# Kernel tuning notes

Hardware: AMD Instinct MI355X
Metric: run time of the kernel (lower is better)

## Reference

```python
import jax, jax.numpy as jnp
import numpy as np

N_HEADS = 16

def setup_inputs() -> dict:
    key = jax.random.key(0)
    ks = jax.random.split(key, 5)
    C = 1024
    B, T = 2, 2048
    s_in = 1.0 / np.sqrt(C)
    x = jax.random.normal(ks[0], (B, T, C), dtype=jnp.float32)
    W_qkv = jax.random.normal(ks[1], (C, 3 * C), dtype=jnp.float32) * s_in
    b_qkv = jnp.zeros((3 * C,), dtype=jnp.float32)
    W_proj = jax.random.normal(ks[2], (C, C), dtype=jnp.float32) * s_in
    b_proj = jnp.zeros((C,), dtype=jnp.float32)
    return {"x": x, "W_qkv": W_qkv, "b_qkv": b_qkv, "W_proj": W_proj, "b_proj": b_proj}

def reference(x, W_qkv, b_qkv, W_proj, b_proj):
    B, T, C = x.shape
    H = N_HEADS
    D = C // H  # head dim
    qkv = x @ W_qkv + b_qkv                      # [B,T,3C]
    q, k, v = jnp.split(qkv, 3, axis=-1)
    # [B,T,C] -> [B,H,T,D]
    q = q.reshape(B, T, H, D).transpose(0, 2, 1, 3)
    k = k.reshape(B, T, H, D).transpose(0, 2, 1, 3)
    v = v.reshape(B, T, H, D).transpose(0, 2, 1, 3)
    scale = 1.0 / np.sqrt(D)
    att = jnp.einsum('bhqd,bhkd->bhqk', q, k) * scale  # [B,H,T,T]
    causal = jnp.tril(jnp.ones((T, T), dtype=bool))
    att = jnp.where(causal[None, None], att, -jnp.inf)
    att = jax.nn.softmax(att, axis=-1)
    y = jnp.einsum('bhqk,bhkd->bhqd', att, v)    # [B,H,T,D]
    y = y.transpose(0, 2, 1, 3).reshape(B, T, C)
    return y @ W_proj + b_proj
```

## Files before the change

kernel.cpp:

```cpp
#include <hip/hip_runtime.h>
#include <hip/hip_bf16.h>
#include <stdint.h>

#define DEVI __device__ __forceinline__

#define BARRIER_FENCED() asm volatile("s_barrier" ::: "memory")
#define WAIT_VM_BARRIER(n) \
  asm volatile("s_waitcnt vmcnt(" #n ")\n\ts_barrier" ::: "memory")

typedef __attribute__((ext_vector_type(8))) short bf16x8;
typedef __attribute__((ext_vector_type(4))) float f32x4;
typedef __attribute__((ext_vector_type(4))) short short4v;
typedef __attribute__((ext_vector_type(4))) float float4v;
typedef __attribute__((ext_vector_type(2))) unsigned int uint2v;

#define QSCALE 0.1803368801111204f

DEVI unsigned short f2bf(float f) {
  union { float f; unsigned u; } v; v.f = f;
  unsigned r = v.u + 0x7FFFu + ((v.u >> 16) & 1u);
  return (unsigned short)(r >> 16);
}

DEVI float bf2f(unsigned short u) {
  union { unsigned u; float f; } v; v.u = ((unsigned)u) << 16; return v.f;
}

DEVI unsigned cvt_pk_bf16(float lo, float hi) {
  unsigned r;
  asm("v_cvt_pk_bf16_f32 %0, %1, %2" : "=v"(r) : "v"(lo), "v"(hi));
  return r;
}

DEVI void async16(unsigned short* lds, const unsigned short* g) {
  __builtin_amdgcn_global_load_lds(
      (const __attribute__((address_space(1))) void*)g,
      (__attribute__((address_space(3))) void*)lds, 16, 0, 0);
}

DEVI int xcd_swz_flat() {
  int orig = (int)blockIdx.x + (int)gridDim.x * (int)blockIdx.y;
  int cpx = ((int)gridDim.x * (int)gridDim.y) >> 3;
  return (orig & 7) * cpx + (orig >> 3);
}

__device__ const signed char TTX[8][3] = {
  {15,15, 0},{ 7,13, 1},{14,12, 2},{14,10, 3},
  {13,10, 8},{ 6, 9, 9},{12,11, 8},{11, 5, 4}};
__device__ const signed char TTS[8][3] = {
  {0,1,2},{2,0,2},{0,0,2},{1,0,2},{1,1,0},{2,0,1},{1,0,1},{1,2,2}};

__global__ void k_prep(const float* __restrict__ x, unsigned short* __restrict__ xb,
                       const float* __restrict__ Wq, const float* __restrict__ Wp,
                       unsigned short* __restrict__ WqT, unsigned short* __restrict__ WpT) {
  __shared__ float tile[32][33];
  const int id = (int)blockIdx.x;
  if (id < 4096) {
    int i = id * 256 + (int)threadIdx.x;
    float4v f = *reinterpret_cast<const float4v*>(x + (size_t)i * 4);
    short4v o;
#pragma unroll
    for (int j = 0; j < 4; ++j) o[j] = (short)f2bf(f[j]);
    *reinterpret_cast<short4v*>(xb + (size_t)i * 4) = o;
    return;
  }
  const int flat = id - 4096;
  const int bx = flat & 127, k0 = (flat >> 7) * 32;
  const float* W;
  unsigned short* Wt;
  int N, n0;
  if (bx < 96) { W = Wq; Wt = WqT; N = 3072; n0 = bx * 32; }
  else         { W = Wp; Wt = WpT; N = 1024; n0 = (bx - 96) * 32; }
  const int K = 1024;
  int r = threadIdx.x >> 5, c = threadIdx.x & 31;
#pragma unroll
  for (int i = 0; i < 4; ++i)
    tile[r + i * 8][c] = W[(size_t)(k0 + r + i * 8) * N + n0 + c];
  __syncthreads();
#pragma unroll
  for (int i = 0; i < 4; ++i)
    Wt[(size_t)(n0 + r + i * 8) * K + k0 + c] = f2bf(tile[c][r + i * 8]);
}

DEVI void stage_ab(unsigned short* AsB, unsigned short* BsB,
                   const unsigned short* Ab, const unsigned short* Bb,
                   int K, int k0, int tid) {
  int row = tid >> 2, cc = (tid & 3) * 8;
  async16(&AsB[tid * 8], Ab + (size_t)row * K + k0 + cc);
  async16(&BsB[tid * 8], Bb + (size_t)row * K + k0 + cc);
}

__global__ __launch_bounds__(512)
void k_gemm(const unsigned short* __restrict__ A,
            const unsigned short* __restrict__ Bt,
            const float* __restrict__ bias,
            unsigned short* __restrict__ qkv,
            unsigned short* __restrict__ vt,
            int M, int N, int K) {
  __shared__ __align__(16) unsigned short As[2][128 * 32];
  __shared__ __align__(16) unsigned short Bs[2][128 * 32];
  const int tid = threadIdx.x;
  const int swzf = xcd_swz_flat();
  const int m0 = (swzf / (int)gridDim.x) * 128, n0 = (swzf % (int)gridDim.x) * 128;
  const int lane = tid & 63, w = tid >> 6;
  const int wr = (w >> 2) * 64, wc = (w & 3) * 32;
  const int lr = lane & 15, lg = lane >> 4;
  f32x4 acc[4][2] = {};
  const unsigned short* Ab = A + (size_t)m0 * K;
  const unsigned short* Bb = Bt + (size_t)n0 * K;

  const int ns = K >> 5;
  stage_ab(As[0], Bs[0], Ab, Bb, K, 0, tid);
  stage_ab(As[1], Bs[1], Ab, Bb, K, 32, tid);
  WAIT_VM_BARRIER(2);
  __builtin_amdgcn_sched_barrier(0);

  for (int s = 0; s < ns; ++s) {
    const int cur = s & 1;
    bf16x8 af[4], bfr[2];
#pragma unroll
    for (int m = 0; m < 4; ++m)
      af[m] = *reinterpret_cast<const bf16x8*>(&As[cur][(wr + m * 16 + lr) * 32 + lg * 8]);
#pragma unroll
    for (int n = 0; n < 2; ++n)
      bfr[n] = *reinterpret_cast<const bf16x8*>(&Bs[cur][(wc + n * 16 + lr) * 32 + lg * 8]);
#pragma unroll
    for (int m = 0; m < 4; ++m)
#pragma unroll
      for (int n = 0; n < 2; ++n)
        acc[m][n] = __builtin_amdgcn_mfma_f32_16x16x32_bf16(af[m], bfr[n], acc[m][n], 0, 0, 0);
    BARRIER_FENCED();
    const int ks = (s + 2 < ns) ? (s + 2) * 32 : 0;
    stage_ab(As[cur], Bs[cur], Ab, Bb, K, ks, tid);
    WAIT_VM_BARRIER(2);
    __builtin_amdgcn_sched_barrier(0);
  }
#pragma unroll
  for (int n = 0; n < 2; ++n) {
    int col = n0 + wc + n * 16 + lr;
    float bv = bias[col];
    int sel = col >> 10, cc = col & 1023;
    int h = cc >> 6, d = cc & 63;
    if (sel < 2) {
      float sc = (sel == 0) ? QSCALE : 1.0f;
#pragma unroll
      for (int m = 0; m < 4; ++m) {
#pragma unroll
        for (int r = 0; r < 4; ++r) {
          int row = m0 + wr + m * 16 + lg * 4 + r;
          int bh = ((row >> 11) << 4) + h;
          int t = row & 2047;
          qkv[((size_t)(sel * 32 + bh) * 2048 + t) * 64 + d] = f2bf((acc[m][n][r] + bv) * sc);
        }
      }
    } else {
#pragma unroll
      for (int m = 0; m < 4; ++m) {
        int row0 = m0 + wr + m * 16 + lg * 4;
        int bh = ((row0 >> 11) << 4) + h;
        int t0 = row0 & 2047;
        short4v pk;
#pragma unroll
        for (int r = 0; r < 4; ++r) pk[r] = (short)f2bf(acc[m][n][r] + bv);
        *reinterpret_cast<short4v*>(&vt[((size_t)(bh * 64 + d)) * 2048 + t0]) = pk;
      }
    }
  }
}

__global__ __launch_bounds__(256)
void k_gemmP(const unsigned short* __restrict__ A,
             const unsigned short* __restrict__ Bt,
             const float* __restrict__ bias,
             float* __restrict__ O, int M, int N, int K) {
  __shared__ __align__(16) unsigned short As[2][64 * 32];
  __shared__ __align__(16) unsigned short Bs[2][64 * 32];
  const int tid = threadIdx.x;
  const int swzf = xcd_swz_flat();
  const int m0 = (swzf / (int)gridDim.x) * 64, n0 = (swzf % (int)gridDim.x) * 64;
  const int lane = tid & 63, w = tid >> 6;
  const int wr = (w >> 1) * 32, wc = (w & 1) * 32;
  const int lr = lane & 15, lg = lane >> 4;
  f32x4 acc[2][2] = {};
  const unsigned short* Ab = A + (size_t)m0 * K;
  const unsigned short* Bb = Bt + (size_t)n0 * K;

  auto stage = [&](unsigned short* AsB, unsigned short* BsB, int k0) {
    int row = tid >> 2, cc = (tid & 3) * 8;
    async16(&AsB[tid * 8], Ab + (size_t)row * K + k0 + cc);
    async16(&BsB[tid * 8], Bb + (size_t)row * K + k0 + cc);
  };

  const int ns = K >> 5;
  stage(As[0], Bs[0], 0);
  stage(As[1], Bs[1], 32);
  WAIT_VM_BARRIER(2);
  __builtin_amdgcn_sched_barrier(0);

  for (int s = 0; s < ns; ++s) {
    const int cur = s & 1;
    bf16x8 af[2], bfr[2];
#pragma unroll
    for (int m = 0; m < 2; ++m)
      af[m] = *reinterpret_cast<const bf16x8*>(&As[cur][(wr + m * 16 + lr) * 32 + lg * 8]);
#pragma unroll
    for (int n = 0; n < 2; ++n)
      bfr[n] = *reinterpret_cast<const bf16x8*>(&Bs[cur][(wc + n * 16 + lr) * 32 + lg * 8]);
#pragma unroll
    for (int m = 0; m < 2; ++m)
#pragma unroll
      for (int n = 0; n < 2; ++n)
        acc[m][n] = __builtin_amdgcn_mfma_f32_16x16x32_bf16(af[m], bfr[n], acc[m][n], 0, 0, 0);
    BARRIER_FENCED();
    const int ks = (s + 2 < ns) ? (s + 2) * 32 : 0;
    stage(As[cur], Bs[cur], ks);
    WAIT_VM_BARRIER(2);
    __builtin_amdgcn_sched_barrier(0);
  }
#pragma unroll
  for (int n = 0; n < 2; ++n) {
    int col = n0 + wc + n * 16 + lr;
    float bv = bias[col];
#pragma unroll
    for (int m = 0; m < 2; ++m)
#pragma unroll
      for (int r = 0; r < 4; ++r) {
        int row = m0 + wr + m * 16 + lg * 4 + r;
        O[(size_t)row * N + col] = acc[m][n][r] + bv;
      }
  }
}

DEVI void stage_kv(unsigned short* KsB, unsigned short* VsB,
                   const unsigned short* Kbh, const unsigned short* Vbh,
                   int k0, int tid, int srow, int gcol) {
  async16(&KsB[tid * 8], Kbh + (size_t)(k0 + srow) * 64 + gcol);
  async16(&VsB[tid * 8], Vbh + (size_t)srow * 2048 + k0 + gcol);
}

__global__ __launch_bounds__(512)
void k_attn(const unsigned short* __restrict__ Qg,
            const unsigned short* __restrict__ Kg,
            const unsigned short* __restrict__ Vtg,
            unsigned short* __restrict__ Y,
            unsigned short* __restrict__ po,
            float2* __restrict__ pml) {
  __shared__ __align__(16) unsigned short Ks[2][64 * 64];
  __shared__ __align__(16) unsigned short Vs[2][64 * 64];
  __shared__ __align__(16) unsigned short Ps[8][16 * 64];
  const int orig = (int)blockIdx.x;
  const int xcd = orig & 7;
  const int p = orig >> 3;
  const int slot = p >> 5;
  const int q = p & 31;
  const int type = q >> 2, cpy = q & 3;
  const int bh = xcd * 4 + ((cpy + slot) & 3);
  const int x = TTX[type][slot];
  const int sf = TTS[type][slot];
  const int nsplit = (sf == 2) ? 1 : 2;
  const int s = (sf == 2) ? 0 : sf;
  const int tA = (nsplit == 2 && s == 1) ? (x + 1) : 0;
  const int tB = (nsplit == 2 && s == 0) ? (x + 1) : (2 * x + 2);
  const int tid = threadIdx.x, lane = tid & 63, w = tid >> 6;
  const int lr = lane & 15, lg = lane >> 4;
  const int swz = (lane & 7) * 8;
  const int psw = (lr & 7) * 8;
  const unsigned short* Kbh = Kg + (size_t)bh * 2048 * 64;
  const unsigned short* Vbh = Vtg + (size_t)bh * 64 * 2048;

  const int qw = x * 128 + w * 16;
  const unsigned short* Qrow = Qg + ((size_t)bh * 2048 + qw + lr) * 64;
  bf16x8 qa0 = *reinterpret_cast<const bf16x8*>(&Qrow[lg * 8]);
  bf16x8 qa1 = *reinterpret_cast<const bf16x8*>(&Qrow[32 + lg * 8]);

  float l_run = 0.f;
  f32x4 o[4] = {};

  const int srow = tid >> 3;
  const int gcol = ((tid & 7) ^ (srow & 7)) * 8;

  stage_kv(Ks[0], Vs[0], Kbh, Vbh, tA * 64, tid, srow, gcol);
  stage_kv(Ks[1], Vs[1], Kbh, Vbh, (tA + 1) * 64, tid, srow, gcol);
  WAIT_VM_BARRIER(2);
  __builtin_amdgcn_sched_barrier(0);

  for (int t = tA; t < tB; ++t) {
    const int cur = (t - tA) & 1;
    const int k0 = t * 64;
    if (k0 <= qw + 15) {
      const unsigned short* KsC = Ks[cur];
      const unsigned short* VsC = Vs[cur];

      f32x4 sc[4];
      __builtin_amdgcn_s_setprio(1);
#pragma unroll
      for (int n = 0; n < 4; ++n) {
        bf16x8 kb0 = *reinterpret_cast<const bf16x8*>(&KsC[(n * 16 + lr) * 64 + ((lg * 8) ^ swz)]);
        bf16x8 kb1 = *reinterpret_cast<const bf16x8*>(&KsC[(n * 16 + lr) * 64 + ((32 + lg * 8) ^ swz)]);
        f32x4 z = {0.f, 0.f, 0.f, 0.f};
        z = __builtin_amdgcn_mfma_f32_16x16x32_bf16(kb0, qa0, z, 0, 0, 0);
        z = __builtin_amdgcn_mfma_f32_16x16x32_bf16(kb1, qa1, z, 0, 0, 0);
        sc[n] = z;
      }
      __builtin_amdgcn_s_setprio(0);
      if (k0 + 63 > qw) {
        const int klim = qw + lr - k0 - lg * 4;
#pragma unroll
        for (int n = 0; n < 4; ++n)
#pragma unroll
          for (int r = 0; r < 4; ++r)
            if (n * 16 + r > klim) sc[n][r] = -1e30f;
      }
#pragma unroll
      for (int n = 0; n < 4; ++n)
#pragma unroll
        for (int r = 0; r < 4; ++r) {
          sc[n][r] = __builtin_exp2f(sc[n][r]);
          l_run += sc[n][r];
        }
#pragma unroll
      for (int n = 0; n < 4; ++n) {
        uint2v pk;
        pk[0] = cvt_pk_bf16(sc[n][0], sc[n][1]);
        pk[1] = cvt_pk_bf16(sc[n][2], sc[n][3]);
        *reinterpret_cast<uint2v*>(&Ps[w][lr * 64 + ((n * 16 + lg * 4) ^ psw)]) = pk;
      }
      __builtin_amdgcn_s_setprio(1);
#pragma unroll
      for (int jj = 0; jj < 2; ++jj) {
        bf16x8 pa = *reinterpret_cast<const bf16x8*>(&Ps[w][lr * 64 + ((jj * 32 + lg * 8) ^ psw)]);
#pragma unroll
        for (int n = 0; n < 4; ++n) {
          bf16x8 vb = *reinterpret_cast<const bf16x8*>(
              &VsC[(n * 16 + lr) * 64 + ((jj * 32 + lg * 8) ^ swz)]);
          o[n] = __builtin_amdgcn_mfma_f32_16x16x32_bf16(pa, vb, o[n], 0, 0, 0);
        }
      }
      __builtin_amdgcn_s_setprio(0);
    }
    BARRIER_FENCED();
    {
      const int ts = (t + 2 < tB) ? (t + 2) : tA;
      stage_kv(Ks[cur], Vs[cur], Kbh, Vbh, ts * 64, tid, srow, gcol);
    }
    WAIT_VM_BARRIER(2);
    __builtin_amdgcn_sched_barrier(0);
  }
  l_run += __shfl_xor(l_run, 16, 64);
  l_run += __shfl_xor(l_run, 32, 64);
  const int b = bh >> 4, h = bh & 15;
  if (nsplit == 1) {
    float rl = 1.0f / l_run;
    float rlo[4];
#pragma unroll
    for (int r = 0; r < 4; ++r) rlo[r] = __shfl(rl, lg * 4 + r, 64);
#pragma unroll
    for (int r = 0; r < 4; ++r) {
      int t = qw + lg * 4 + r;
#pragma unroll
      for (int n = 0; n < 4; ++n)
        Y[((size_t)(b * 2048 + t)) * 1024 + h * 64 + n * 16 + lr] = f2bf(o[n][r] * rlo[r]);
    }
  } else {
    const int g = bh * 8 + (x - 8);
    if (lg == 0) {
      float2 v; v.x = 0.f; v.y = l_run;
      pml[(g * 2 + s) * 128 + w * 16 + lr] = v;
    }
    float oo[4][4];
#pragma unroll
    for (int r = 0; r < 4; ++r)
#pragma unroll
      for (int n = 0; n < 4; ++n) oo[r][n] = o[n][r];
    if (s == 0) {
#pragma unroll
      for (int r = 0; r < 4; ++r) {
        int t = qw + lg * 4 + r;
#pragma unroll
        for (int n = 0; n < 4; ++n)
          Y[((size_t)(b * 2048 + t)) * 1024 + h * 64 + n * 16 + lr] = f2bf(oo[r][n]);
      }
    } else {
#pragma unroll
      for (int r = 0; r < 4; ++r) {
        int row = w * 16 + lg * 4 + r;
#pragma unroll
        for (int n = 0; n < 4; ++n)
          po[((size_t)g * 128 + row) * 64 + n * 16 + lr] = f2bf(oo[r][n]);
      }
    }
  }
}

__global__ __launch_bounds__(256)
void k_merge(unsigned short* __restrict__ Y,
             const unsigned short* __restrict__ po,
             const float2* __restrict__ pml) {
  const int g = (int)blockIdx.x;
  const int bh = g >> 3, x = (g & 7) + 8;
  const int b = bh >> 4, h = bh & 15;
  const int row = threadIdx.x >> 1;
  const int d0 = ((int)threadIdx.x & 1) * 32;
  float2 p0 = pml[(g * 2 + 0) * 128 + row];
  float2 p1 = pml[(g * 2 + 1) * 128 + row];
  float m = fmaxf(p0.x, p1.x);
  float a0 = __builtin_exp2f(p0.x - m), a1 = __builtin_exp2f(p1.x - m);
  float inv = 1.0f / (p0.y * a0 + p1.y * a1);
  float c0 = a0 * inv, c1 = a1 * inv;
  size_t yb = ((size_t)(b * 2048 + x * 128 + row)) * 1024 + h * 64 + d0;
  size_t pb = ((size_t)g * 128 + row) * 64 + d0;
#pragma unroll
  for (int i = 0; i < 4; ++i) {
    bf16x8 yv = *reinterpret_cast<const bf16x8*>(&Y[yb + i * 8]);
    bf16x8 pv = *reinterpret_cast<const bf16x8*>(&po[pb + i * 8]);
    bf16x8 ov;
#pragma unroll
    for (int jj = 0; jj < 8; ++jj)
      ov[jj] = (short)f2bf(bf2f((unsigned short)yv[jj]) * c0 +
                           bf2f((unsigned short)pv[jj]) * c1);
    *reinterpret_cast<bf16x8*>(&Y[yb + i * 8]) = ov;
  }
}

extern "C" void kernel_launch(void* const* d_in, const int* in_sizes, int n_in,
                              void* d_out, int out_size, void* d_ws, size_t ws_size,
                              hipStream_t stream) {
  const float* x     = (const float*)d_in[0];
  const float* Wqkv  = (const float*)d_in[1];
  const float* bqkv  = (const float*)d_in[2];
  const float* Wproj = (const float*)d_in[3];
  const float* bproj = (const float*)d_in[4];
  float* out = (float*)d_out;

  uint8_t* ws = (uint8_t*)d_ws;
  unsigned short* xb     = (unsigned short*)(ws);
  unsigned short* wqkvT  = (unsigned short*)(ws + ((size_t)8  << 20));
  unsigned short* wprojT = (unsigned short*)(ws + ((size_t)14 << 20));
  unsigned short* qkvb   = (unsigned short*)(ws + ((size_t)16 << 20));
  unsigned short* vt     = (unsigned short*)(ws + ((size_t)32 << 20));
  unsigned short* po     = (unsigned short*)(ws + ((size_t)8  << 20));
  float2*         pml    = (float2*)(ws + ((size_t)12 << 20));

  k_prep<<<dim3(8192, 1), 256, 0, stream>>>(x, xb, Wqkv, Wproj, wqkvT, wprojT);
  k_gemm<<<dim3(24, 32), 512, 0, stream>>>(xb, wqkvT, bqkv, qkvb, vt, 4096, 3072, 1024);
  k_attn<<<dim3(768, 1), 512, 0, stream>>>(qkvb, qkvb + (size_t)32 * 2048 * 64, vt, xb, po, pml);
  k_merge<<<dim3(256, 1), 256, 0, stream>>>(xb, po, pml);
  k_gemmP<<<dim3(16, 64), 256, 0, stream>>>(xb, wprojT, bproj, out, 4096, 1024, 1024);
}
```

Measured before the change: 104.3 us.

## Switch GEMM and attention pipelines to one-ahead prefetch with single barrier

```diff
diff --git a/kernel.cpp b/kernel.cpp
--- a/kernel.cpp
+++ b/kernel.cpp
@@ -4,9 +4,8 @@
 
 #define DEVI __device__ __forceinline__
 
-#define BARRIER_FENCED() asm volatile("s_barrier" ::: "memory")
-#define WAIT_VM_BARRIER(n) \
-  asm volatile("s_waitcnt vmcnt(" #n ")\n\ts_barrier" ::: "memory")
+#define WAIT_VM0_BARRIER() \
+  asm volatile("s_waitcnt vmcnt(0)\n\ts_barrier" ::: "memory")
 
 typedef __attribute__((ext_vector_type(8))) short bf16x8;
 typedef __attribute__((ext_vector_type(4))) float f32x4;
@@ -111,12 +110,13 @@
 
   const int ns = K >> 5;
   stage_ab(As[0], Bs[0], Ab, Bb, K, 0, tid);
-  stage_ab(As[1], Bs[1], Ab, Bb, K, 32, tid);
-  WAIT_VM_BARRIER(2);
+  WAIT_VM0_BARRIER();
   __builtin_amdgcn_sched_barrier(0);
 
   for (int s = 0; s < ns; ++s) {
     const int cur = s & 1;
+    if (s + 1 < ns)
+      stage_ab(As[cur ^ 1], Bs[cur ^ 1], Ab, Bb, K, (s + 1) * 32, tid);
     bf16x8 af[4], bfr[2];
 #pragma unroll
     for (int m = 0; m < 4; ++m)
@@ -129,10 +129,7 @@
 #pragma unroll
       for (int n = 0; n < 2; ++n)
         acc[m][n] = __builtin_amdgcn_mfma_f32_16x16x32_bf16(af[m], bfr[n], acc[m][n], 0, 0, 0);
-    BARRIER_FENCED();
-    const int ks = (s + 2 < ns) ? (s + 2) * 32 : 0;
-    stage_ab(As[cur], Bs[cur], Ab, Bb, K, ks, tid);
-    WAIT_VM_BARRIER(2);
+    WAIT_VM0_BARRIER();
     __builtin_amdgcn_sched_barrier(0);
   }
 #pragma unroll
@@ -193,12 +190,13 @@
 
   const int ns = K >> 5;
   stage(As[0], Bs[0], 0);
-  stage(As[1], Bs[1], 32);
-  WAIT_VM_BARRIER(2);
+  WAIT_VM0_BARRIER();
   __builtin_amdgcn_sched_barrier(0);
 
   for (int s = 0; s < ns; ++s) {
     const int cur = s & 1;
+    if (s + 1 < ns)
+      stage(As[cur ^ 1], Bs[cur ^ 1], (s + 1) * 32);
     bf16x8 af[2], bfr[2];
 #pragma unroll
     for (int m = 0; m < 2; ++m)
@@ -211,10 +209,7 @@
 #pragma unroll
       for (int n = 0; n < 2; ++n)
         acc[m][n] = __builtin_amdgcn_mfma_f32_16x16x32_bf16(af[m], bfr[n], acc[m][n], 0, 0, 0);
-    BARRIER_FENCED();
-    const int ks = (s + 2 < ns) ? (s + 2) * 32 : 0;
-    stage(As[cur], Bs[cur], ks);
-    WAIT_VM_BARRIER(2);
+    WAIT_VM0_BARRIER();
     __builtin_amdgcn_sched_barrier(0);
   }
 #pragma unroll
@@ -280,12 +275,13 @@
   const int gcol = ((tid & 7) ^ (srow & 7)) * 8;
 
   stage_kv(Ks[0], Vs[0], Kbh, Vbh, tA * 64, tid, srow, gcol);
-  stage_kv(Ks[1], Vs[1], Kbh, Vbh, (tA + 1) * 64, tid, srow, gcol);
-  WAIT_VM_BARRIER(2);
+  WAIT_VM0_BARRIER();
   __builtin_amdgcn_sched_barrier(0);
 
   for (int t = tA; t < tB; ++t) {
     const int cur = (t - tA) & 1;
+    if (t + 1 < tB)
+      stage_kv(Ks[cur ^ 1], Vs[cur ^ 1], Kbh, Vbh, (t + 1) * 64, tid, srow, gcol);
     const int k0 = t * 64;
     if (k0 <= qw + 15) {
       const unsigned short* KsC = Ks[cur];
@@ -338,12 +334,7 @@
       }
       __builtin_amdgcn_s_setprio(0);
     }
-    BARRIER_FENCED();
-    {
-      const int ts = (t + 2 < tB) ? (t + 2) : tA;
-      stage_kv(Ks[cur], Vs[cur], Kbh, Vbh, ts * 64, tid, srow, gcol);
-    }
-    WAIT_VM_BARRIER(2);
+    WAIT_VM0_BARRIER();
     __builtin_amdgcn_sched_barrier(0);
   }
   l_run += __shfl_xor(l_run, 16, 64);
```

Result: no change. 102.7 us (-1.5%).
